# Kernel optimization log

Measured on AMD Instinct MI355X. Metric: run time of the kernel, lower is better.

## Reference

```python
import jax, jax.numpy as jnp
import numpy as np

B, N, D, H = 4, 4096, 1024, 16
DH = D // H              # 64
M = int(DH * np.log(DH))  # 266 random features (performer-pytorch default)
EPS = 1e-4


def softmax_kernel(t, proj, is_query):
    # t: [B,H,N,DH], proj: [M,DH]  -> [B,H,N,M]  (FAVOR+ positive features)
    dn = t.shape[-1] ** -0.25
    ratio = proj.shape[0] ** -0.5
    td = jnp.einsum('bhnd,md->bhnm', t * dn, proj)
    diag = 0.5 * (dn ** 2) * jnp.sum(t * t, axis=-1, keepdims=True)  # [B,H,N,1]
    if is_query:
        mx = jnp.max(td, axis=-1, keepdims=True)
    else:
        mx = jnp.max(td, axis=(-1, -2), keepdims=True)
    return ratio * (jnp.exp(td - diag - mx) + EPS)


def setup_inputs() -> dict:
    key = jax.random.key(0)
    ks = jax.random.split(key, 12)
    s = 0.02
    inp = {
        'x':   jax.random.normal(ks[0], (B, N, D), jnp.float32),
        'Wq':  jax.random.normal(ks[1], (D, D), jnp.float32) * s,
        'bq':  jnp.zeros((D,), jnp.float32),
        'Wk':  jax.random.normal(ks[2], (D, D), jnp.float32) * s,
        'bk':  jnp.zeros((D,), jnp.float32),
        'Wv':  jax.random.normal(ks[3], (D, D), jnp.float32) * s,
        'bv':  jnp.zeros((D,), jnp.float32),
        'Wo':  jax.random.normal(ks[4], (D, D), jnp.float32) * s,
        'bo':  jnp.zeros((D,), jnp.float32),
        'Wfc': jax.random.normal(ks[5], (D, D), jnp.float32) * s,
        'bfc': jnp.zeros((D,), jnp.float32),
        'proj': jax.random.normal(ks[6], (M, DH), jnp.float32),  # random feature projection (frozen)
    }
    return inp


def reference(x, Wq, bq, Wk, bk, Wv, bv, Wo, bo, Wfc, bfc, proj):
    b, n, d = x.shape
    def heads(t):  # [B,N,D] -> [B,H,N,DH]
        return t.reshape(b, n, H, DH).transpose(0, 2, 1, 3)
    q = heads(x @ Wq.T + bq)
    k = heads(x @ Wk.T + bk)
    v = heads(x @ Wv.T + bv)

    qp = softmax_kernel(q, proj, is_query=True)    # [B,H,N,M]
    kp = softmax_kernel(k, proj, is_query=False)   # [B,H,N,M]

    # non-causal linear attention: O(N*M*DH)
    k_sum = jnp.sum(kp, axis=-2)                               # [B,H,M]
    d_inv = 1.0 / jnp.einsum('bhnm,bhm->bhn', qp, k_sum)       # [B,H,N]
    context = jnp.einsum('bhnm,bhnd->bhmd', kp, v)             # [B,H,M,DH]
    out = jnp.einsum('bhmd,bhnm,bhn->bhnd', context, qp, d_inv)

    out = out.transpose(0, 2, 1, 3).reshape(b, n, d)           # merge heads
    h = out @ Wo.T + bo                                        # performer internal to_out
    return jax.nn.relu(h @ Wfc.T + bfc)                        # wrapper fc_out + ReLU
```

## Files before the change

### kernel.cpp

```cpp
#include <hip/hip_runtime.h>
#include <math.h>

#define B_ 4
#define N_ 4096
#define D_ 1024
#define H_ 16
#define DH_ 64
#define M_ 266
#define MP_ 320

#define DN_ 0.35355339059327373f
#define RATIO_ 0.06131393394849658f
#define EPS_ 1e-4f
#define KP_ 72
#define NSPLIT_ 16
#define PARTSZ_ ((size_t)64 * M_ * 64)

typedef __attribute__((ext_vector_type(8))) short bfrag;
typedef __attribute__((ext_vector_type(4))) float f4;

__device__ __forceinline__ unsigned f2ord(float f) {
    unsigned u = __float_as_uint(f);
    return (u & 0x80000000u) ? ~u : (u | 0x80000000u);
}
__device__ __forceinline__ float ord2f(unsigned u) {
    unsigned b = (u & 0x80000000u) ? (u & 0x7fffffffu) : ~u;
    return __uint_as_float(b);
}

__global__ void zero_kernel(float* __restrict__ p, int n) {
    int i = blockIdx.x * 256 + threadIdx.x;
    if (i < n) p[i] = 0.f;
}

__device__ __forceinline__ void split2pack(float x, float y, unsigned* hp, unsigned* lp) {
    unsigned ux = __float_as_uint(x), uy = __float_as_uint(y);
    float hx = __uint_as_float(ux & 0xffff0000u);
    float hy = __uint_as_float(uy & 0xffff0000u);
    float lx = x - hx, ly = y - hy;
    *hp = (ux >> 16) | (uy & 0xffff0000u);
    *lp = (__float_as_uint(lx) >> 16) | (__float_as_uint(ly) & 0xffff0000u);
}
__device__ __forceinline__ unsigned short bf16rne(float x) {
    unsigned u = __float_as_uint(x);
    return (unsigned short)((u + 0x7fffu + ((u >> 16) & 1u)) >> 16);
}

__device__ __forceinline__ void async_cp16(const void* g, void* l) {
    __builtin_amdgcn_global_load_lds(
        (const __attribute__((address_space(1))) void*)g,
        (__attribute__((address_space(3))) void*)l, 16, 0, 0);
}

__global__ __launch_bounds__(256) void split_f32(const float* __restrict__ X,
        unsigned short* __restrict__ Xh, unsigned short* __restrict__ Xl, int n4)
{
    int i = blockIdx.x * 256 + threadIdx.x;
    if (i >= n4) return;
    const float4 v = ((const float4*)X)[i];
    unsigned h0, l0, h1, l1;
    split2pack(v.x, v.y, &h0, &l0);
    split2pack(v.z, v.w, &h1, &l1);
    ((uint2*)Xh)[i] = make_uint2(h0, h1);
    ((uint2*)Xl)[i] = make_uint2(l0, l1);
}

__global__ __launch_bounds__(256) void split_w5(const float* __restrict__ W0,
        const float* __restrict__ W1, const float* __restrict__ W2,
        const float* __restrict__ W3, const float* __restrict__ W4,
        unsigned short* __restrict__ Wsp)
{
    int sel = blockIdx.y;
    const float* W = (sel == 0) ? W0 : (sel == 1) ? W1 : (sel == 2) ? W2 : (sel == 3) ? W3 : W4;
    unsigned short* h = Wsp + (size_t)sel * 2097152;
    unsigned short* l = h + 1048576;
    int i = blockIdx.x * 256 + threadIdx.x;
    const float4 v = ((const float4*)W)[i];
    unsigned h0, l0, h1, l1;
    split2pack(v.x, v.y, &h0, &l0);
    split2pack(v.z, v.w, &h1, &l1);
    ((uint2*)h)[i] = make_uint2(h0, h1);
    ((uint2*)l)[i] = make_uint2(l0, l1);
}

__global__ __launch_bounds__(256) void presplit_proj(const float* __restrict__ proj,
        unsigned short* __restrict__ projR, unsigned short* __restrict__ projHg,
        unsigned short* __restrict__ projLg)
{
    int i = blockIdx.x * 256 + threadIdx.x;
    int m = i >> 6, d = i & 63;
    float v = (m < M_) ? proj[m * 64 + d] : 0.f;
    projR[i] = bf16rne(v);
    unsigned u = __float_as_uint(v);
    float lo = v - __uint_as_float(u & 0xffff0000u);
    projHg[i] = (unsigned short)(u >> 16);
    projLg[i] = (unsigned short)(__float_as_uint(lo) >> 16);
}

__global__ __launch_bounds__(256) void gemm_qkv_s(
        const unsigned short* __restrict__ Ah, const unsigned short* __restrict__ Al,
        const unsigned short* __restrict__ Wsp,
        const float* __restrict__ b0, const float* __restrict__ b1, const float* __restrict__ b2,
        float* __restrict__ C0, float* __restrict__ C1, float* __restrict__ C2)
{
    __shared__ __align__(16) unsigned short Ahs[128 * 32];
    __shared__ __align__(16) unsigned short Als[128 * 32];
    __shared__ __align__(16) unsigned short Bhs[128 * 32];
    __shared__ __align__(16) unsigned short Bls[128 * 32];

    int tid = threadIdx.x;
    int sel = blockIdx.x >> 3;
    int bn = (blockIdx.x & 7) * 128;
    int bm = blockIdx.y * 128;
    const unsigned short* Bh = Wsp + (size_t)sel * 2097152;
    const unsigned short* Bl = Bh + 1048576;
    const float* bias = (sel == 0) ? b0 : (sel == 1) ? b1 : b2;
    float* C = (sel == 0) ? C0 : (sel == 1) ? C1 : C2;

    int lane = tid & 63;
    int w = tid >> 6;
    int wm = w >> 1, wn = w & 1;
    int ml = lane & 15, kq = lane >> 4;
    int rsub = lane >> 2;
    int ksw = (((lane & 3) ^ ((lane >> 3) & 3))) * 8;
    int slot8 = ((kq ^ ((ml >> 1) & 3))) * 8;

    f4 acc[4][4];
    #pragma unroll
    for (int i = 0; i < 4; ++i)
        #pragma unroll
        for (int j = 0; j < 4; ++j)
            acc[i][j] = (f4){0.f, 0.f, 0.f, 0.f};

    for (int kt = 0; kt < D_; kt += 32) {
        __syncthreads();
        #pragma unroll
        for (int j = 0; j < 2; ++j) {
            int row = w * 32 + j * 16;
            size_t ga = (size_t)(bm + row + rsub) * D_ + kt + ksw;
            size_t gb = (size_t)(bn + row + rsub) * D_ + kt + ksw;
            async_cp16(Ah + ga, &Ahs[row * 32]);
            async_cp16(Al + ga, &Als[row * 32]);
            async_cp16(Bh + gb, &Bhs[row * 32]);
            async_cp16(Bl + gb, &Bls[row * 32]);
        }
        __syncthreads();
        bfrag ah[4], al[4], bh[4], bl[4];
        #pragma unroll
        for (int i = 0; i < 4; ++i) {
            int arow = wm * 64 + i * 16 + ml;
            ah[i] = *(const bfrag*)&Ahs[arow * 32 + slot8];
            al[i] = *(const bfrag*)&Als[arow * 32 + slot8];
            int brow = wn * 64 + i * 16 + ml;
            bh[i] = *(const bfrag*)&Bhs[brow * 32 + slot8];
            bl[i] = *(const bfrag*)&Bls[brow * 32 + slot8];
        }
        #pragma unroll
        for (int mi = 0; mi < 4; ++mi)
            #pragma unroll
            for (int ni = 0; ni < 4; ++ni) {
                acc[mi][ni] = __builtin_amdgcn_mfma_f32_16x16x32_bf16(ah[mi], bh[ni], acc[mi][ni], 0, 0, 0);
                acc[mi][ni] = __builtin_amdgcn_mfma_f32_16x16x32_bf16(al[mi], bh[ni], acc[mi][ni], 0, 0, 0);
                acc[mi][ni] = __builtin_amdgcn_mfma_f32_16x16x32_bf16(ah[mi], bl[ni], acc[mi][ni], 0, 0, 0);
            }
    }
    #pragma unroll
    for (int ni = 0; ni < 4; ++ni) {
        int col = bn + wn * 64 + ni * 16 + ml;
        float bv = bias[col];
        #pragma unroll
        for (int mi = 0; mi < 4; ++mi) {
            int row0 = bm + wm * 64 + mi * 16 + kq * 4;
            #pragma unroll
            for (int r = 0; r < 4; ++r)
                C[(size_t)(row0 + r) * D_ + col] = acc[mi][ni][r] + bv;
        }
    }
}

__global__ __launch_bounds__(256) void gemm_nt_s(
        const unsigned short* __restrict__ Ah, const unsigned short* __restrict__ Al,
        const unsigned short* __restrict__ Bh, const unsigned short* __restrict__ Bl,
        const float* __restrict__ bias, float* __restrict__ C,
        unsigned short* __restrict__ Ch, unsigned short* __restrict__ Cl, int mode)
{
    __shared__ __align__(16) unsigned short Ahs[128 * 32];
    __shared__ __align__(16) unsigned short Als[128 * 32];
    __shared__ __align__(16) unsigned short Bhs[128 * 32];
    __shared__ __align__(16) unsigned short Bls[128 * 32];

    int tid = threadIdx.x;
    int bn = blockIdx.x * 128;
    int bm = blockIdx.y * 128;
    int lane = tid & 63;
    int w = tid >> 6;
    int wm = w >> 1, wn = w & 1;
    int ml = lane & 15, kq = lane >> 4;
    int rsub = lane >> 2;
    int ksw = (((lane & 3) ^ ((lane >> 3) & 3))) * 8;
    int slot8 = ((kq ^ ((ml >> 1) & 3))) * 8;

    f4 acc[4][4];
    #pragma unroll
    for (int i = 0; i < 4; ++i)
        #pragma unroll
        for (int j = 0; j < 4; ++j)
            acc[i][j] = (f4){0.f, 0.f, 0.f, 0.f};

    for (int kt = 0; kt < D_; kt += 32) {
        __syncthreads();
        #pragma unroll
        for (int j = 0; j < 2; ++j) {
            int row = w * 32 + j * 16;
            size_t ga = (size_t)(bm + row + rsub) * D_ + kt + ksw;
            size_t gb = (size_t)(bn + row + rsub) * D_ + kt + ksw;
            async_cp16(Ah + ga, &Ahs[row * 32]);
            async_cp16(Al + ga, &Als[row * 32]);
            async_cp16(Bh + gb, &Bhs[row * 32]);
            async_cp16(Bl + gb, &Bls[row * 32]);
        }
        __syncthreads();
        bfrag ah[4], al[4], bh[4], bl[4];
        #pragma unroll
        for (int i = 0; i < 4; ++i) {
            int arow = wm * 64 + i * 16 + ml;
            ah[i] = *(const bfrag*)&Ahs[arow * 32 + slot8];
            al[i] = *(const bfrag*)&Als[arow * 32 + slot8];
            int brow = wn * 64 + i * 16 + ml;
            bh[i] = *(const bfrag*)&Bhs[brow * 32 + slot8];
            bl[i] = *(const bfrag*)&Bls[brow * 32 + slot8];
        }
        #pragma unroll
        for (int mi = 0; mi < 4; ++mi)
            #pragma unroll
            for (int ni = 0; ni < 4; ++ni) {
                acc[mi][ni] = __builtin_amdgcn_mfma_f32_16x16x32_bf16(ah[mi], bh[ni], acc[mi][ni], 0, 0, 0);
                acc[mi][ni] = __builtin_amdgcn_mfma_f32_16x16x32_bf16(al[mi], bh[ni], acc[mi][ni], 0, 0, 0);
                acc[mi][ni] = __builtin_amdgcn_mfma_f32_16x16x32_bf16(ah[mi], bl[ni], acc[mi][ni], 0, 0, 0);
            }
    }
    #pragma unroll
    for (int ni = 0; ni < 4; ++ni) {
        int col = bn + wn * 64 + ni * 16 + ml;
        float bv = bias[col];
        #pragma unroll
        for (int mi = 0; mi < 4; ++mi) {
            int row0 = bm + wm * 64 + mi * 16 + kq * 4;
            #pragma unroll
            for (int r = 0; r < 4; ++r) {
                float o = acc[mi][ni][r] + bv;
                size_t idx = (size_t)(row0 + r) * D_ + col;
                if (mode == 2) {
                    unsigned u = __float_as_uint(o);
                    float lo = o - __uint_as_float(u & 0xffff0000u);
                    Ch[idx] = (unsigned short)(u >> 16);
                    Cl[idx] = (unsigned short)(__float_as_uint(lo) >> 16);
                } else {
                    if (mode == 1) o = fmaxf(o, 0.f);
                    C[idx] = o;
                }
            }
        }
    }
}

__global__ __launch_bounds__(256) void kside(
    const float* __restrict__ Kin, const float* __restrict__ Vin,
    const unsigned short* __restrict__ projR,
    float* __restrict__ S_u, float* __restrict__ Cpart, float* __restrict__ C_u,
    float* __restrict__ Vsum, unsigned int* __restrict__ mxp)
{
    __shared__ __align__(16) unsigned short Kh[64 * KP_];
    __shared__ __align__(16) unsigned short VT[64 * KP_];
    __shared__ __align__(16) unsigned short Ph[2][64 * KP_];
    __shared__ __align__(16) unsigned short Us[64 * KP_];
    __shared__ __align__(16) float Ssum[MP_];
    __shared__ float diag[64];
    float* redf = (float*)Us;

    int bh = blockIdx.y, b = bh >> 4, h = bh & 15;
    int s = blockIdx.x;
    int n0 = s * 256;
    int tid = threadIdx.x, lane = tid & 63, w = tid >> 6;
    int ml = lane & 15, quad = lane >> 4;

    float* dstC = (s < NSPLIT_ - 1) ? (Cpart + (size_t)s * PARTSZ_) : C_u;

    for (int i = tid; i < MP_; i += 256) Ssum[i] = 0.f;

    f4 acc[5][4];
    #pragma unroll
    for (int i = 0; i < 5; ++i)
        #pragma unroll
        for (int j = 0; j < 4; ++j) acc[i][j] = (f4){0.f, 0.f, 0.f, 0.f};
    float vs[4] = {0.f, 0.f, 0.f, 0.f};
    float lmax = -1e30f;

    for (int nc = 0; nc < 4; ++nc) {
        __syncthreads();
        #pragma unroll
        for (int l = 0; l < 4; ++l) {
            int idx = tid + 256 * l;
            int r = idx >> 4;
            int d4 = (idx & 15) * 4;
            size_t g = ((size_t)(b * N_ + n0 + nc * 64 + r)) * D_ + h * DH_ + d4;
            const float4 kv = *(const float4*)(Kin + g);
            redf[r * 17 + (tid & 15)] = kv.x * kv.x + kv.y * kv.y + kv.z * kv.z + kv.w * kv.w;
            unsigned w0 = (unsigned)bf16rne(kv.x * DN_) | ((unsigned)bf16rne(kv.y * DN_) << 16);
            unsigned w1 = (unsigned)bf16rne(kv.z * DN_) | ((unsigned)bf16rne(kv.w * DN_) << 16);
            *(uint2*)&Kh[r * KP_ + d4] = make_uint2(w0, w1);
            const float4 vv = *(const float4*)(Vin + g);
            vs[0] += vv.x; vs[1] += vv.y; vs[2] += vv.z; vs[3] += vv.w;
            VT[(d4 + 0) * KP_ + r] = bf16rne(vv.x);
            VT[(d4 + 1) * KP_ + r] = bf16rne(vv.y);
            VT[(d4 + 2) * KP_ + r] = bf16rne(vv.z);
            VT[(d4 + 3) * KP_ + r] = bf16rne(vv.w);
        }
        {
            #pragma unroll
            for (int l = 0; l < 2; ++l) {
                int idx = tid + 256 * l;
                int m = idx >> 3, d8 = (idx & 7) * 8;
                *(uint4*)&Ph[0][m * KP_ + d8] = *(const uint4*)(projR + m * 64 + d8);
            }
        }
        __syncthreads();
        if (tid < 64) {
            float ss = 0.f;
            #pragma unroll
            for (int p = 0; p < 16; ++p) ss += redf[tid * 17 + p];
            diag[tid] = ss * 0.0625f;
        }
        __syncthreads();

        bfrag kh0 = *(const bfrag*)&Kh[(w * 16 + ml) * KP_ + quad * 8];
        bfrag kh1 = *(const bfrag*)&Kh[(w * 16 + ml) * KP_ + 32 + quad * 8];
        float dgv[4];
        #pragma unroll
        for (int r = 0; r < 4; ++r) dgv[r] = diag[w * 16 + quad * 4 + r];

        for (int mc = 0; mc < 5; ++mc) {
            int pb = mc & 1;
            uint4 pf2[2];
            if (mc < 4) {
                #pragma unroll
                for (int l = 0; l < 2; ++l) {
                    int idx = tid + 256 * l;
                    int m = idx >> 3, d8 = (idx & 7) * 8;
                    int mg = (mc + 1) * 64 + m;
                    pf2[l] = *(const uint4*)(projR + mg * 64 + d8);
                }
            }
            #pragma unroll
            for (int mt = 0; mt < 4; ++mt) {
                int mrow = mt * 16 + ml;
                bfrag ph0 = *(const bfrag*)&Ph[pb][mrow * KP_ + quad * 8];
                bfrag ph1 = *(const bfrag*)&Ph[pb][mrow * KP_ + 32 + quad * 8];
                f4 t = (f4){0.f, 0.f, 0.f, 0.f};
                t = __builtin_amdgcn_mfma_f32_16x16x32_bf16(kh0, ph0, t, 0, 0, 0);
                t = __builtin_amdgcn_mfma_f32_16x16x32_bf16(kh1, ph1, t, 0, 0, 0);
                bool mv = (mc * 64 + mrow) < M_;
                float su = 0.f;
                unsigned short up[4];
                #pragma unroll
                for (int r = 0; r < 4; ++r) {
                    float u = 0.f;
                    if (mv) {
                        float tt = t[r];
                        lmax = fmaxf(lmax, tt);
                        u = __expf(tt - dgv[r]);
                    }
                    su += u;
                    up[r] = bf16rne(u);
                }
                su += __shfl_xor(su, 16);
                su += __shfl_xor(su, 32);
                if (mv && quad == 0) atomicAdd(&Ssum[mc * 64 + mrow], su);
                unsigned w0 = (unsigned)up[0] | ((unsigned)up[1] << 16);
                unsigned w1 = (unsigned)up[2] | ((unsigned)up[3] << 16);
                *(uint2*)&Us[mrow * KP_ + w * 16 + quad * 4] = make_uint2(w0, w1);
            }
            if (mc < 4) {
                #pragma unroll
                for (int l = 0; l < 2; ++l) {
                    int idx = tid + 256 * l;
                    int m = idx >> 3, d8 = (idx & 7) * 8;
                    *(uint4*)&Ph[1 - pb][m * KP_ + d8] = pf2[l];
                }
            }
            __syncthreads();
            bfrag ua0 = *(const bfrag*)&Us[(w * 16 + ml) * KP_ + quad * 8];
            bfrag ua1 = *(const bfrag*)&Us[(w * 16 + ml) * KP_ + 32 + quad * 8];
            #pragma unroll
            for (int dt = 0; dt < 4; ++dt) {
                bfrag vb0 = *(const bfrag*)&VT[(dt * 16 + ml) * KP_ + quad * 8];
                bfrag vb1 = *(const bfrag*)&VT[(dt * 16 + ml) * KP_ + 32 + quad * 8];
                acc[mc][dt] = __builtin_amdgcn_mfma_f32_16x16x32_bf16(ua0, vb0, acc[mc][dt], 0, 0, 0);
                acc[mc][dt] = __builtin_amdgcn_mfma_f32_16x16x32_bf16(ua1, vb1, acc[mc][dt], 0, 0, 0);
            }
            __syncthreads();
        }
    }
    #pragma unroll
    for (int mc = 0; mc < 5; ++mc)
        #pragma unroll
        for (int dt = 0; dt < 4; ++dt)
            #pragma unroll
            for (int r = 0; r < 4; ++r) {
                int m = mc * 64 + w * 16 + quad * 4 + r;
                if (m < M_)
                    dstC[((size_t)bh * M_ + m) * 64 + dt * 16 + ml] = acc[mc][dt][r];
            }
    __syncthreads();
    for (int m = tid; m < M_; m += 256)
        atomicAdd(S_u + bh * M_ + m, Ssum[m]);
    #pragma unroll
    for (int off = 32; off; off >>= 1) lmax = fmaxf(lmax, __shfl_xor(lmax, off));
    __syncthreads();
    if (lane == 0) redf[w] = lmax;
    __syncthreads();
    if (tid == 0) {
        float mxv = fmaxf(fmaxf(redf[0], redf[1]), fmaxf(redf[2], redf[3]));
        atomicMax(mxp + bh, f2ord(mxv));
    }
    for (int j = 0; j < 4; ++j) {
        __syncthreads();
        redf[tid] = vs[j];
        __syncthreads();
        if (tid < 16) {
            float ss = 0.f;
            #pragma unroll
            for (int p = 0; p < 16; ++p) ss += redf[tid + 16 * p];
            atomicAdd(Vsum + bh * 64 + tid * 4 + j, ss);
        }
    }
}

__global__ __launch_bounds__(256) void finalize_kernel(
    const float* __restrict__ S_u, const float* __restrict__ Cpart, const float* __restrict__ C_u,
    const float* __restrict__ Vsum, const unsigned* __restrict__ mxp,
    float* __restrict__ ksum_f, unsigned short* __restrict__ ctxTh,
    unsigned short* __restrict__ ctxTl, float* __restrict__ Cs, float* __restrict__ kss)
{
    __shared__ float T[64 * 65];
    __shared__ float red[256];
    int mc = blockIdx.x, bh = blockIdx.y;
    int tid = threadIdx.x;
    float emx = __expf(-ord2f(mxp[bh]));

    float csacc = 0.f;
    #pragma unroll
    for (int i = 0; i < 16; ++i) {
        int idx = i * 256 + tid;
        int dh = idx & 63, mloc = idx >> 6;
        int m = mc * 64 + mloc;
        float v = 0.f;
        if (m < M_) {
            size_t off = ((size_t)bh * M_ + m) * 64 + dh;
            float sacc = C_u[off];
            for (int sp = 0; sp < NSPLIT_ - 1; ++sp)
                sacc += Cpart[(size_t)sp * PARTSZ_ + off];
            v = RATIO_ * (emx * sacc + EPS_ * Vsum[bh * 64 + dh]);
        }
        T[mloc * 65 + dh] = v;
        csacc += v;
    }
    red[tid] = csacc;
    __syncthreads();
    if (tid < 64) atomicAdd(&Cs[bh * 64 + tid], red[tid] + red[tid + 64] + red[tid + 128] + red[tid + 192]);
    float ksl = 0.f;
    if (tid < 64) {
        int m = mc * 64 + tid;
        float kv = (m < M_) ? RATIO_ * (emx * S_u[bh * M_ + m] + EPS_ * (float)N_) : 0.f;
        ksum_f[bh * MP_ + m] = kv;
        ksl = kv;
    }
    __syncthreads();
    red[tid] = ksl;
    __syncthreads();
    if (tid == 0) {
        float ss = 0.f;
        for (int p = 0; p < 64; ++p) ss += red[p];
        atomicAdd(kss + bh, ss);
    }
    __syncthreads();
    #pragma unroll
    for (int i = 0; i < 8; ++i) {
        int idx = i * 256 + tid;
        int dh = idx >> 5, m2 = (idx & 31) * 2;
        float v0 = T[m2 * 65 + dh], v1 = T[(m2 + 1) * 65 + dh];
        unsigned u0 = __float_as_uint(v0), u1 = __float_as_uint(v1);
        float lo0 = v0 - __uint_as_float(u0 & 0xffff0000u);
        float lo1 = v1 - __uint_as_float(u1 & 0xffff0000u);
        size_t dst = ((size_t)(bh * 64 + dh)) * MP_ + mc * 64 + m2;
        *(unsigned*)&ctxTh[dst] = (u0 >> 16) | (u1 & 0xffff0000u);
        *(unsigned*)&ctxTl[dst] = (__float_as_uint(lo0) >> 16) | (__float_as_uint(lo1) & 0xffff0000u);
    }
}

__global__ __launch_bounds__(256) void qattn(
    const float* __restrict__ Q, const unsigned short* __restrict__ projHg,
    const unsigned short* __restrict__ projLg,
    const float* __restrict__ ksum_f, const unsigned short* __restrict__ ctxTh,
    const unsigned short* __restrict__ ctxTl,
    const float* __restrict__ Cs, const float* __restrict__ kss,
    unsigned short* __restrict__ attnH, unsigned short* __restrict__ attnL)
{
    __shared__ __align__(16) unsigned short Qh[64 * KP_], Ql[64 * KP_];
    __shared__ __align__(16) unsigned short Ph[64 * KP_], Pl[64 * KP_];
    __shared__ __align__(16) unsigned short Uh[64 * KP_], Ul[64 * KP_];
    __shared__ __align__(16) float ks[MP_];
    __shared__ float diag[64];
    float* redf = (float*)Uh;

    int bh = blockIdx.y, b = bh >> 4, h = bh & 15;
    int n0 = blockIdx.x * 64;
    int tid = threadIdx.x, lane = tid & 63, w = tid >> 6;
    int ml = lane & 15, quad = lane >> 4;

    #pragma unroll
    for (int l = 0; l < 4; ++l) {
        int idx = tid + 256 * l;
        int r = idx >> 4, d4 = (idx & 15) * 4;
        size_t g = ((size_t)(b * N_ + n0 + r)) * D_ + h * DH_ + d4;
        const float4 qv = *(const float4*)(Q + g);
        redf[r * 17 + (tid & 15)] = qv.x * qv.x + qv.y * qv.y + qv.z * qv.z + qv.w * qv.w;
        unsigned h0, l0, h1, l1;
        split2pack(qv.x * DN_, qv.y * DN_, &h0, &l0);
        split2pack(qv.z * DN_, qv.w * DN_, &h1, &l1);
        *(uint2*)&Qh[r * KP_ + d4] = make_uint2(h0, h1);
        *(uint2*)&Ql[r * KP_ + d4] = make_uint2(l0, l1);
    }
    for (int m = tid; m < MP_; m += 256) ks[m] = ksum_f[bh * MP_ + m];
    __syncthreads();
    if (tid < 64) {
        float s = 0.f;
        #pragma unroll
        for (int p = 0; p < 16; ++p) s += redf[tid * 17 + p];
        diag[tid] = s * 0.0625f;
    }
    __syncthreads();

    bfrag qh0 = *(const bfrag*)&Qh[(w * 16 + ml) * KP_ + quad * 8];
    bfrag ql0 = *(const bfrag*)&Ql[(w * 16 + ml) * KP_ + quad * 8];
    bfrag qh1 = *(const bfrag*)&Qh[(w * 16 + ml) * KP_ + 32 + quad * 8];
    bfrag ql1 = *(const bfrag*)&Ql[(w * 16 + ml) * KP_ + 32 + quad * 8];
    float dg = diag[w * 16 + ml];
    float dacc = 0.f, tmax = -1e30f;
    f4 oacc[4];
    #pragma unroll
    for (int i = 0; i < 4; ++i) oacc[i] = (f4){0.f, 0.f, 0.f, 0.f};

    for (int mc = 0; mc < 5; ++mc) {
        #pragma unroll
        for (int l = 0; l < 2; ++l) {
            int idx = tid + 256 * l;
            int m = idx >> 3, d8 = (idx & 7) * 8;
            int mg = mc * 64 + m;
            *(uint4*)&Ph[m * KP_ + d8] = *(const uint4*)(projHg + mg * 64 + d8);
            *(uint4*)&Pl[m * KP_ + d8] = *(const uint4*)(projLg + mg * 64 + d8);
        }
        __syncthreads();
        #pragma unroll
        for (int mt = 0; mt < 4; ++mt) {
            int mrow = mt * 16 + ml;
            bfrag ph0 = *(const bfrag*)&Ph[mrow * KP_ + quad * 8];
            bfrag pl0 = *(const bfrag*)&Pl[mrow * KP_ + quad * 8];
            bfrag ph1 = *(const bfrag*)&Ph[mrow * KP_ + 32 + quad * 8];
            bfrag pl1 = *(const bfrag*)&Pl[mrow * KP_ + 32 + quad * 8];
            f4 t = (f4){0.f, 0.f, 0.f, 0.f};
            t = __builtin_amdgcn_mfma_f32_16x16x32_bf16(ph0, qh0, t, 0, 0, 0);
            t = __builtin_amdgcn_mfma_f32_16x16x32_bf16(pl0, qh0, t, 0, 0, 0);
            t = __builtin_amdgcn_mfma_f32_16x16x32_bf16(ph0, ql0, t, 0, 0, 0);
            t = __builtin_amdgcn_mfma_f32_16x16x32_bf16(ph1, qh1, t, 0, 0, 0);
            t = __builtin_amdgcn_mfma_f32_16x16x32_bf16(pl1, qh1, t, 0, 0, 0);
            t = __builtin_amdgcn_mfma_f32_16x16x32_bf16(ph1, ql1, t, 0, 0, 0);
            const float4 ksv = *(const float4*)&ks[mc * 64 + mt * 16 + quad * 4];
            float ksa[4] = {ksv.x, ksv.y, ksv.z, ksv.w};
            unsigned short uh4[4], ul4[4];
            #pragma unroll
            for (int r = 0; r < 4; ++r) {
                int mg = mc * 64 + mt * 16 + quad * 4 + r;
                float tt = t[r];
                float u = __expf(tt - dg);
                if (mg < M_) tmax = fmaxf(tmax, tt);
                dacc = fmaf(u, ksa[r], dacc);
                unsigned uu = __float_as_uint(u);
                float lo = u - __uint_as_float(uu & 0xffff0000u);
                uh4[r] = (unsigned short)(uu >> 16);
                ul4[r] = (unsigned short)(__float_as_uint(lo) >> 16);
            }
            unsigned a0 = (unsigned)uh4[0] | ((unsigned)uh4[1] << 16);
            unsigned a1 = (unsigned)uh4[2] | ((unsigned)uh4[3] << 16);
            unsigned b0 = (unsigned)ul4[0] | ((unsigned)ul4[1] << 16);
            unsigned b1 = (unsigned)ul4[2] | ((unsigned)ul4[3] << 16);
            *(uint2*)&Uh[(w * 16 + ml) * KP_ + mt * 16 + quad * 4] = make_uint2(a0, a1);
            *(uint2*)&Ul[(w * 16 + ml) * KP_ + mt * 16 + quad * 4] = make_uint2(b0, b1);
        }
        __syncthreads();
        #pragma unroll
        for (int l = 0; l < 2; ++l) {
            int idx = tid + 256 * l;
            int dh = idx >> 3, m8 = (idx & 7) * 8;
            size_t src = ((size_t)(bh * 64 + dh)) * MP_ + mc * 64 + m8;
            *(uint4*)&Ph[dh * KP_ + m8] = *(const uint4*)(ctxTh + src);
            *(uint4*)&Pl[dh * KP_ + m8] = *(const uint4*)(ctxTl + src);
        }
        __syncthreads();
        bfrag ua0h = *(const bfrag*)&Uh[(w * 16 + ml) * KP_ + quad * 8];
        bfrag ua0l = *(const bfrag*)&Ul[(w * 16 + ml) * KP_ + quad * 8];
        bfrag ua1h = *(const bfrag*)&Uh[(w * 16 + ml) * KP_ + 32 + quad * 8];
        bfrag ua1l = *(const bfrag*)&Ul[(w * 16 + ml) * KP_ + 32 + quad * 8];
        #pragma unroll
        for (int dt = 0; dt < 4; ++dt) {
            bfrag cb0h = *(const bfrag*)&Ph[(dt * 16 + ml) * KP_ + quad * 8];
            bfrag cb0l = *(const bfrag*)&Pl[(dt * 16 + ml) * KP_ + quad * 8];
            bfrag cb1h = *(const bfrag*)&Ph[(dt * 16 + ml) * KP_ + 32 + quad * 8];
            bfrag cb1l = *(const bfrag*)&Pl[(dt * 16 + ml) * KP_ + 32 + quad * 8];
            oacc[dt] = __builtin_amdgcn_mfma_f32_16x16x32_bf16(ua0h, cb0h, oacc[dt], 0, 0, 0);
            oacc[dt] = __builtin_amdgcn_mfma_f32_16x16x32_bf16(ua0l, cb0h, oacc[dt], 0, 0, 0);
            oacc[dt] = __builtin_amdgcn_mfma_f32_16x16x32_bf16(ua0h, cb0l, oacc[dt], 0, 0, 0);
            oacc[dt] = __builtin_amdgcn_mfma_f32_16x16x32_bf16(ua1h, cb1h, oacc[dt], 0, 0, 0);
            oacc[dt] = __builtin_amdgcn_mfma_f32_16x16x32_bf16(ua1l, cb1h, oacc[dt], 0, 0, 0);
            oacc[dt] = __builtin_amdgcn_mfma_f32_16x16x32_bf16(ua1h, cb1l, oacc[dt], 0, 0, 0);
        }
        __syncthreads();
    }
    dacc += __shfl_xor(dacc, 16); dacc += __shfl_xor(dacc, 32);
    tmax = fmaxf(tmax, __shfl_xor(tmax, 16));
    tmax = fmaxf(tmax, __shfl_xor(tmax, 32));
    float fac = EPS_ * __expf(tmax);
    float dinv = 1.f / (dacc + fac * kss[bh]);
    #pragma unroll
    for (int dt = 0; dt < 4; ++dt) {
        float csv = Cs[bh * 64 + dt * 16 + ml];
        #pragma unroll
        for (int r = 0; r < 4; ++r) {
            int srcl = quad * 4 + r;
            float dv = __shfl(dinv, srcl);
            float fv = __shfl(fac, srcl);
            float o = (oacc[dt][r] + fv * csv) * dv;
            int n = n0 + w * 16 + quad * 4 + r;
            size_t gi = ((size_t)(b * N_ + n)) * D_ + h * DH_ + dt * 16 + ml;
            unsigned u = __float_as_uint(o);
            float lo = o - __uint_as_float(u & 0xffff0000u);
            attnH[gi] = (unsigned short)(u >> 16);
            attnL[gi] = (unsigned short)(__float_as_uint(lo) >> 16);
        }
    }
}

extern "C" void kernel_launch(void* const* d_in, const int* in_sizes, int n_in,
                              void* d_out, int out_size, void* d_ws, size_t ws_size,
                              hipStream_t stream)
{
    const float* x    = (const float*)d_in[0];
    const float* Wq   = (const float*)d_in[1];
    const float* bq   = (const float*)d_in[2];
    const float* Wk   = (const float*)d_in[3];
    const float* bk   = (const float*)d_in[4];
    const float* Wv   = (const float*)d_in[5];
    const float* bv   = (const float*)d_in[6];
    const float* Wo   = (const float*)d_in[7];
    const float* bo   = (const float*)d_in[8];
    const float* Wfc  = (const float*)d_in[9];
    const float* bfc  = (const float*)d_in[10];
    const float* proj = (const float*)d_in[11];
    float* out = (float*)d_out;

    float* ws = (float*)d_ws;
    const size_t nTok = (size_t)B_ * N_ * D_;
    const size_t nSu  = 64 * M_;
    const size_t nCu  = (size_t)64 * M_ * 64;
    const size_t nVs  = 64 * 64;
    const size_t nMx  = 64;
    const size_t nKsf = 64 * MP_;
    const size_t nCtx = (size_t)64 * MP_ * 64;
    const size_t nCs  = 64 * 64;

    const size_t offQ   = 0;
    const size_t offK   = nTok;
    const size_t offV   = nTok * 2;
    const size_t offSu  = nTok * 3;
    const size_t offCu  = offSu + nSu;
    const size_t offVs  = offCu + nCu;
    const size_t offMx  = offVs + nVs;
    const size_t offKsf = offMx + nMx;
    const size_t offCtx = offKsf + nKsf;
    const size_t offCs  = offCtx + nCtx;
    const size_t offKss = offCs + nCs;
    const size_t offWsp = offKss + 64;
    const size_t offPrj = offWsp + 5242880;

    float* Q    = ws + offQ;
    float* Kb   = ws + offK;
    float* Vb   = ws + offV;
    float* S_u  = ws + offSu;
    float* C_u  = ws + offCu;
    float* Vsum = ws + offVs;
    unsigned* mx = (unsigned*)(ws + offMx);
    float* ksf  = ws + offKsf;
    unsigned short* ctxTh = (unsigned short*)(ws + offCtx);
    unsigned short* ctxTl = ctxTh + (size_t)64 * 64 * MP_;
    float* Cs   = ws + offCs;
    float* kss  = ws + offKss;
    unsigned short* Wsp = (unsigned short*)(ws + offWsp);
    unsigned short* projR  = (unsigned short*)(ws + offPrj);
    unsigned short* projHg = projR + (size_t)MP_ * 64;
    unsigned short* projLg = projHg + (size_t)MP_ * 64;

    unsigned short* xh = (unsigned short*)out;
    unsigned short* xl = xh + nTok;
    unsigned short* attnH = (unsigned short*)Kb;
    unsigned short* attnL = attnH + nTok;
    unsigned short* hbH = (unsigned short*)Vb;
    unsigned short* hbL = hbH + nTok;
    float* Cpart = out;

    int nzero = (int)(nSu + nCu + nVs + nMx + nKsf + nCtx + nCs + 64);
    zero_kernel<<<dim3((nzero + 255) / 256), dim3(256), 0, stream>>>(S_u, nzero);

    split_f32<<<dim3(16384), dim3(256), 0, stream>>>(x, xh, xl, (int)(nTok / 4));
    split_w5<<<dim3(1024, 5), dim3(256), 0, stream>>>(Wq, Wk, Wv, Wo, Wfc, Wsp);
    presplit_proj<<<dim3(80), dim3(256), 0, stream>>>(proj, projR, projHg, projLg);

    gemm_qkv_s<<<dim3(24, (B_ * N_) / 128), dim3(256), 0, stream>>>(
        xh, xl, Wsp, bq, bk, bv, Q, Kb, Vb);

    kside<<<dim3(NSPLIT_, 64), dim3(256), 0, stream>>>(Kb, Vb, projR, S_u, Cpart, C_u, Vsum, mx);
    finalize_kernel<<<dim3(5, 64), dim3(256), 0, stream>>>(S_u, Cpart, C_u, Vsum, mx, ksf, ctxTh, ctxTl, Cs, kss);
    qattn<<<dim3(64, 64), dim3(256), 0, stream>>>(Q, projHg, projLg, ksf, ctxTh, ctxTl, Cs, kss, attnH, attnL);

    dim3 gg(D_ / 128, (B_ * N_) / 128);
    gemm_nt_s<<<gg, dim3(256), 0, stream>>>(attnH, attnL,
        Wsp + (size_t)3 * 2097152, Wsp + (size_t)3 * 2097152 + 1048576,
        bo, (float*)nullptr, hbH, hbL, 2);
    gemm_nt_s<<<gg, dim3(256), 0, stream>>>(hbH, hbL,
        Wsp + (size_t)4 * 2097152, Wsp + (size_t)4 * 2097152 + 1048576,
        bfc, out, (unsigned short*)nullptr, (unsigned short*)nullptr, 1);
}
```

Measured before the change: 988.1 us.

## Prefetch ctx and proj tiles into registers to overlap loads with MFMA

In qattn, the context tile now gets its own shared buffers (Chs/Cls), so the proj and ctx tiles no longer share Ph/Pl. Each chunk's ctx loads are issued into registers before the feature-map MFMAs, and the next chunk's proj tile is fetched during the output MFMAs. This cuts the syncthreads per iteration from four to two and hides global load latency behind compute. It adds shared memory and register pressure, which may lower occupancy.

New measurement: 970.4 us (median of 2 runs). About the same (-1.8%).

```diff
diff --git a/kernel.cpp b/kernel.cpp
--- a/kernel.cpp
+++ b/kernel.cpp
@@ -508,6 +508,7 @@
 {
     __shared__ __align__(16) unsigned short Qh[64 * KP_], Ql[64 * KP_];
     __shared__ __align__(16) unsigned short Ph[64 * KP_], Pl[64 * KP_];
+    __shared__ __align__(16) unsigned short Chs[64 * KP_], Cls[64 * KP_];
     __shared__ __align__(16) unsigned short Uh[64 * KP_], Ul[64 * KP_];
     __shared__ __align__(16) float ks[MP_];
     __shared__ float diag[64];
@@ -531,6 +532,13 @@
         *(uint2*)&Qh[r * KP_ + d4] = make_uint2(h0, h1);
         *(uint2*)&Ql[r * KP_ + d4] = make_uint2(l0, l1);
     }
+    #pragma unroll
+    for (int l = 0; l < 2; ++l) {
+        int idx = tid + 256 * l;
+        int m = idx >> 3, d8 = (idx & 7) * 8;
+        *(uint4*)&Ph[m * KP_ + d8] = *(const uint4*)(projHg + m * 64 + d8);
+        *(uint4*)&Pl[m * KP_ + d8] = *(const uint4*)(projLg + m * 64 + d8);
+    }
     for (int m = tid; m < MP_; m += 256) ks[m] = ksum_f[bh * MP_ + m];
     __syncthreads();
     if (tid < 64) {
@@ -551,16 +559,18 @@
     #pragma unroll
     for (int i = 0; i < 4; ++i) oacc[i] = (f4){0.f, 0.f, 0.f, 0.f};
 
+    int cidx0 = tid, cidx1 = tid + 256;
+    int cdh0 = cidx0 >> 3, cm80 = (cidx0 & 7) * 8;
+    int cdh1 = cidx1 >> 3, cm81 = (cidx1 & 7) * 8;
+
     for (int mc = 0; mc < 5; ++mc) {
-        #pragma unroll
-        for (int l = 0; l < 2; ++l) {
-            int idx = tid + 256 * l;
-            int m = idx >> 3, d8 = (idx & 7) * 8;
-            int mg = mc * 64 + m;
-            *(uint4*)&Ph[m * KP_ + d8] = *(const uint4*)(projHg + mg * 64 + d8);
-            *(uint4*)&Pl[m * KP_ + d8] = *(const uint4*)(projLg + mg * 64 + d8);
-        }
-        __syncthreads();
+        size_t csrc0 = ((size_t)(bh * 64 + cdh0)) * MP_ + mc * 64 + cm80;
+        size_t csrc1 = ((size_t)(bh * 64 + cdh1)) * MP_ + mc * 64 + cm81;
+        uint4 c0 = *(const uint4*)(ctxTh + csrc0);
+        uint4 c1 = *(const uint4*)(ctxTl + csrc0);
+        uint4 c2 = *(const uint4*)(ctxTh + csrc1);
+        uint4 c3 = *(const uint4*)(ctxTl + csrc1);
+
         #pragma unroll
         for (int mt = 0; mt < 4; ++mt) {
             int mrow = mt * 16 + ml;
@@ -597,32 +607,43 @@
             *(uint2*)&Uh[(w * 16 + ml) * KP_ + mt * 16 + quad * 4] = make_uint2(a0, a1);
             *(uint2*)&Ul[(w * 16 + ml) * KP_ + mt * 16 + quad * 4] = make_uint2(b0, b1);
         }
-        __syncthreads();
-        #pragma unroll
-        for (int l = 0; l < 2; ++l) {
-            int idx = tid + 256 * l;
-            int dh = idx >> 3, m8 = (idx & 7) * 8;
-            size_t src = ((size_t)(bh * 64 + dh)) * MP_ + mc * 64 + m8;
-            *(uint4*)&Ph[dh * KP_ + m8] = *(const uint4*)(ctxTh + src);
-            *(uint4*)&Pl[dh * KP_ + m8] = *(const uint4*)(ctxTl + src);
-        }
-        __syncthreads();
+        *(uint4*)&Chs[cdh0 * KP_ + cm80] = c0;
+        *(uint4*)&Cls[cdh0 * KP_ + cm80] = c1;
+        *(uint4*)&Chs[cdh1 * KP_ + cm81] = c2;
+        *(uint4*)&Cls[cdh1 * KP_ + cm81] = c3;
+        __syncthreads();
+
+        uint4 p0, p1, p2, p3;
+        if (mc < 4) {
+            int mg0 = (mc + 1) * 64 + (cidx0 >> 3);
+            int mg1 = (mc + 1) * 64 + (cidx1 >> 3);
+            p0 = *(const uint4*)(projHg + mg0 * 64 + cm80);
+            p1 = *(const uint4*)(projLg + mg0 * 64 + cm80);
+            p2 = *(const uint4*)(projHg + mg1 * 64 + cm81);
+            p3 = *(const uint4*)(projLg + mg1 * 64 + cm81);
+        }
         bfrag ua0h = *(const bfrag*)&Uh[(w * 16 + ml) * KP_ + quad * 8];
         bfrag ua0l = *(const bfrag*)&Ul[(w * 16 + ml) * KP_ + quad * 8];
         bfrag ua1h = *(const bfrag*)&Uh[(w * 16 + ml) * KP_ + 32 + quad * 8];
         bfrag ua1l = *(const bfrag*)&Ul[(w * 16 + ml) * KP_ + 32 + quad * 8];
         #pragma unroll
         for (int dt = 0; dt < 4; ++dt) {
-            bfrag cb0h = *(const bfrag*)&Ph[(dt * 16 + ml) * KP_ + quad * 8];
-            bfrag cb0l = *(const bfrag*)&Pl[(dt * 16 + ml) * KP_ + quad * 8];
-            bfrag cb1h = *(const bfrag*)&Ph[(dt * 16 + ml) * KP_ + 32 + quad * 8];
-            bfrag cb1l = *(const bfrag*)&Pl[(dt * 16 + ml) * KP_ + 32 + quad * 8];
+            bfrag cb0h = *(const bfrag*)&Chs[(dt * 16 + ml) * KP_ + quad * 8];
+            bfrag cb0l = *(const bfrag*)&Cls[(dt * 16 + ml) * KP_ + quad * 8];
+            bfrag cb1h = *(const bfrag*)&Chs[(dt * 16 + ml) * KP_ + 32 + quad * 8];
+            bfrag cb1l = *(const bfrag*)&Cls[(dt * 16 + ml) * KP_ + 32 + quad * 8];
             oacc[dt] = __builtin_amdgcn_mfma_f32_16x16x32_bf16(ua0h, cb0h, oacc[dt], 0, 0, 0);
             oacc[dt] = __builtin_amdgcn_mfma_f32_16x16x32_bf16(ua0l, cb0h, oacc[dt], 0, 0, 0);
             oacc[dt] = __builtin_amdgcn_mfma_f32_16x16x32_bf16(ua0h, cb0l, oacc[dt], 0, 0, 0);
             oacc[dt] = __builtin_amdgcn_mfma_f32_16x16x32_bf16(ua1h, cb1h, oacc[dt], 0, 0, 0);
             oacc[dt] = __builtin_amdgcn_mfma_f32_16x16x32_bf16(ua1l, cb1h, oacc[dt], 0, 0, 0);
             oacc[dt] = __builtin_amdgcn_mfma_f32_16x16x32_bf16(ua1h, cb1l, oacc[dt], 0, 0, 0);
+        }
+        if (mc < 4) {
+            *(uint4*)&Ph[(cidx0 >> 3) * KP_ + cm80] = p0;
+            *(uint4*)&Pl[(cidx0 >> 3) * KP_ + cm80] = p1;
+            *(uint4*)&Ph[(cidx1 >> 3) * KP_ + cm81] = p2;
+            *(uint4*)&Pl[(cidx1 >> 3) * KP_ + cm81] = p3;
         }
         __syncthreads();
     }
```
